# Performance work log

Hardware: AMD Instinct MI355X
Metric: run time of the kernel (lower is better)

The kernel has to match this reference:

```python
import jax, jax.numpy as jnp
import numpy as np

EPS = 1e-5


def gcn_conv(x, W, b, src, dst):
    """PyG GCNConv: transform, add self-loops, symmetric norm, scatter-add, bias."""
    N = x.shape[0]
    h = x @ W  # [N, out]
    loop = jnp.arange(N)
    s = jnp.concatenate([src, loop])  # sources incl. self-loops
    d = jnp.concatenate([dst, loop])  # targets incl. self-loops
    deg = jax.ops.segment_sum(jnp.ones(s.shape[0], h.dtype), d, num_segments=N)
    dis = jnp.where(deg > 0, jax.lax.rsqrt(deg), 0.0)  # deg^-1/2
    norm = dis[s] * dis[d]  # [E+N]
    out = jax.ops.segment_sum(h[s] * norm[:, None], d, num_segments=N)
    return out + b


def batchnorm(x, gamma, beta):
    mu = x.mean(axis=0)
    var = x.var(axis=0)
    return (x - mu) * jax.lax.rsqrt(var + EPS) * gamma + beta


def setup_inputs() -> dict:
    key = jax.random.key(0)
    ks = jax.random.split(key, 6)
    N, E = 100000, 1600000
    IN, HID, OUT = 128, 256, 64
    x = jax.random.normal(ks[0], (N, IN), dtype=jnp.float32)
    edge_index = jax.random.randint(ks[1], (2, E), 0, N, dtype=jnp.int64)
    W1 = jax.random.normal(ks[2], (IN, HID), dtype=jnp.float32) / np.sqrt(IN)
    b1 = jnp.zeros((HID,), jnp.float32)
    gamma1 = jnp.ones((HID,), jnp.float32)
    beta1 = jnp.zeros((HID,), jnp.float32)
    W2 = jax.random.normal(ks[3], (HID, OUT), dtype=jnp.float32) / np.sqrt(HID)
    b2 = jnp.zeros((OUT,), jnp.float32)
    return {"x": x, "edge_index": edge_index, "W1": W1, "b1": b1,
            "gamma1": gamma1, "beta1": beta1, "W2": W2, "b2": b2}


def reference(x, edge_index, W1, b1, gamma1, beta1, W2, b2):
    src, dst = edge_index[0], edge_index[1]
    h = gcn_conv(x, W1, b1, src, dst)
    h = jax.nn.relu(batchnorm(h, gamma1, beta1))
    # dropout is identity at inference
    return gcn_conv(h, W2, b2, src, dst)
```

## Files before the change

kernel.cpp:

```cpp
#include <hip/hip_runtime.h>
#include <hip/hip_bf16.h>


#define IN_F  128
#define HID_F 256
#define OUT_F 64
#define BK_SHIFT 8
#define BK_SIZE  256
#define CHUNK    8192

typedef unsigned int uint;
typedef unsigned short ushort;
typedef short bf16x8 __attribute__((ext_vector_type(8)));
typedef float f32x4 __attribute__((ext_vector_type(4)));

__device__ __forceinline__ ushort f2bf(float f) {
    uint u = __float_as_uint(f);
    uint r = (u + 0x7fffu + ((u >> 16) & 1u)) >> 16;
    return (ushort)r;
}
__device__ __forceinline__ float bf_lo(uint u) { return __uint_as_float(u << 16); }
__device__ __forceinline__ float bf_hi(uint u) { return __uint_as_float(u & 0xffff0000u); }

#define ACC8(u)                                         \
    do {                                                \
        acc[0] += bf_lo((u).x); acc[1] += bf_hi((u).x); \
        acc[2] += bf_lo((u).y); acc[3] += bf_hi((u).y); \
        acc[4] += bf_lo((u).z); acc[5] += bf_hi((u).z); \
        acc[6] += bf_lo((u).w); acc[7] += bf_hi((u).w); \
    } while (0)


__global__ void bucket_hist_kernel(const int* __restrict__ dst, int* __restrict__ bhist,
                                   int E, int NB) {
    __shared__ int h[512];
    for (int i = threadIdx.x; i < NB; i += 256) h[i] = 0;
    __syncthreads();
    int base = blockIdx.x * CHUNK;
    int end = min(base + CHUNK, E);
    for (int i = base + threadIdx.x; i < end; i += 256)
        atomicAdd(&h[dst[i] >> BK_SHIFT], 1);
    __syncthreads();
    for (int i = threadIdx.x; i < NB; i += 256)
        if (h[i]) atomicAdd(&bhist[i], h[i]);
}

__global__ void bucket_scan_kernel(const int* __restrict__ bhist, int* __restrict__ bbase,
                                   int* __restrict__ bcursor, int NB, int E) {
    __shared__ int sh[512];
    int t = threadIdx.x;
    int v = (t < NB) ? bhist[t] : 0;
    sh[t] = v;
    __syncthreads();
    for (int off = 1; off < 512; off <<= 1) {
        int u = (t >= off) ? sh[t - off] : 0;
        __syncthreads();
        sh[t] += u;
        __syncthreads();
    }
    if (t < NB) { int b = sh[t] - v; bbase[t] = b; bcursor[t] = b; }
    if (t == 0) bbase[NB] = E;
}

__global__ void bucket_scatter_kernel(const int* __restrict__ src, const int* __restrict__ dst,
                                      int* __restrict__ bcursor, uint* __restrict__ ebuf,
                                      int E, int NB) {
    __shared__ int h[512];
    __shared__ int cur[512];
    for (int i = threadIdx.x; i < NB; i += 256) h[i] = 0;
    __syncthreads();
    int base = blockIdx.x * CHUNK;
    int end = min(base + CHUNK, E);
    for (int i = base + threadIdx.x; i < end; i += 256)
        atomicAdd(&h[dst[i] >> BK_SHIFT], 1);
    __syncthreads();
    for (int i = threadIdx.x; i < NB; i += 256)
        cur[i] = h[i] ? atomicAdd(&bcursor[i], h[i]) : 0;
    __syncthreads();
    for (int i = base + threadIdx.x; i < end; i += 256) {
        int d = dst[i], s = src[i];
        int b = d >> BK_SHIFT;
        int pos = atomicAdd(&cur[b], 1);
        ebuf[pos] = (uint)s | ((uint)(d & (BK_SIZE - 1)) << 24);
    }
}

__global__ void bucket_build_kernel(const uint* __restrict__ ebuf, const int* __restrict__ bbase,
                                    int* __restrict__ deg_e, int* __restrict__ offsets,
                                    float* __restrict__ dis, int* __restrict__ ssrc, int N) {
    __shared__ int cnt[256], off[256], cur[256];
    int b = blockIdx.x;
    int t = threadIdx.x;
    cnt[t] = 0;
    __syncthreads();
    int e0 = bbase[b], e1 = bbase[b + 1];
    for (int i = e0 + t; i < e1; i += 256)
        atomicAdd(&cnt[ebuf[i] >> 24], 1);
    __syncthreads();
    int v = cnt[t];
    int vpad = (v + 3) & ~3;
    off[t] = vpad;
    __syncthreads();
    for (int o = 1; o < 256; o <<= 1) {
        int u = (t >= o) ? off[t - o] : 0;
        __syncthreads();
        off[t] += u;
        __syncthreads();
    }
    int excl = off[t] - vpad;
    int base_pad = e0 + b * 768;
    int d = b * BK_SIZE + t;
    if (d < N) {
        deg_e[d] = vpad;
        offsets[d] = base_pad + excl;
        dis[d] = rsqrtf((float)(v + 1));
    }
    cur[t] = excl;
    __syncthreads();
    for (int i = e0 + t; i < e1; i += 256) {
        uint e = ebuf[i];
        int ld = e >> 24;
        int pos = atomicAdd(&cur[ld], 1);
        ssrc[base_pad + pos] = (int)(e & 0xFFFFFFu);
    }
    __syncthreads();
    for (int i = v; i < vpad; i++)
        ssrc[base_pad + excl + i] = N;
}

__global__ void prep_kernel(const float* __restrict__ x, const float* __restrict__ dis,
                            uint* __restrict__ xs, const float* __restrict__ W1,
                            const float* __restrict__ W2, ushort* __restrict__ W1bp,
                            ushort* __restrict__ W2bp, int N) {
    int b = blockIdx.x;
    if (b < 192) {
        int i = b * 256 + threadIdx.x;
        if (i < 32768) {
            int kk = i & 31, c = (i >> 5) & 255, kc = i >> 13;
            W1bp[i] = f2bf(W1[(size_t)(kc * 32 + kk) * HID_F + c]);
        } else {
            int j = i - 32768;
            int kk = j & 31, c = (j >> 5) & 63, kc = j >> 11;
            W2bp[j] = f2bf(W2[(size_t)(kc * 32 + kk) * OUT_F + c]);
        }
        return;
    }
    int i = (b - 192) * 256 + threadIdx.x;
    if (i < (N + 1) * (IN_F / 2)) {
        int n = i >> 6;
        if (n >= N) { xs[i] = 0u; return; }
        float dn = dis[n];
        float2 v = ((const float2*)x)[i];
        xs[i] = (uint)f2bf(dn * v.x) | ((uint)f2bf(dn * v.y) << 16);
    }
}


__global__ void aggx_kernel(const uint* __restrict__ xs, const int* __restrict__ ssrc,
                            const int* __restrict__ offsets, const int* __restrict__ deg_e,
                            const float* __restrict__ dis, uint* __restrict__ zb, int N) {
    int lane = threadIdx.x & 63;
    int n = blockIdx.x * 4 + (threadIdx.x >> 6);
    if (n >= N) return;
    int grp = lane >> 4;
    int ck = lane & 15;
    float acc[8];
#pragma unroll
    for (int i = 0; i < 8; i++) acc[i] = 0.f;
    int start = offsets[n], cnt = deg_e[n];
    for (int base = 0; base < cnt; base += 64) {
        int m = min(64, cnt - base);
        int idx = base + lane;
        int sv = ssrc[start + (idx < cnt ? idx : cnt - 1)];
        int rounds = m >> 2;
        int q = 0;
        for (; q + 4 <= rounds; q += 4) {
            int sA = __shfl(sv, ((q + 0) << 2) | grp);
            int sB = __shfl(sv, ((q + 1) << 2) | grp);
            int sC = __shfl(sv, ((q + 2) << 2) | grp);
            int sD = __shfl(sv, ((q + 3) << 2) | grp);
            uint4 uA = *(const uint4*)(xs + ((size_t)sA << 6) + (ck << 2));
            uint4 uB = *(const uint4*)(xs + ((size_t)sB << 6) + (ck << 2));
            uint4 uC = *(const uint4*)(xs + ((size_t)sC << 6) + (ck << 2));
            uint4 uD = *(const uint4*)(xs + ((size_t)sD << 6) + (ck << 2));
            ACC8(uA); ACC8(uB); ACC8(uC); ACC8(uD);
        }
        for (; q < rounds; q++) {
            int s = __shfl(sv, (q << 2) | grp);
            uint4 u = *(const uint4*)(xs + ((size_t)s << 6) + (ck << 2));
            ACC8(u);
        }
    }
#pragma unroll
    for (int i = 0; i < 8; i++) acc[i] += __shfl_down(acc[i], 32);
#pragma unroll
    for (int i = 0; i < 8; i++) acc[i] += __shfl_down(acc[i], 16);
    if (grp == 0) {
        uint4 u = *(const uint4*)(xs + ((size_t)n << 6) + (ck << 2));
        ACC8(u);
        float dn = dis[n];
        uint4 o;
        o.x = (uint)f2bf(dn * acc[0]) | ((uint)f2bf(dn * acc[1]) << 16);
        o.y = (uint)f2bf(dn * acc[2]) | ((uint)f2bf(dn * acc[3]) << 16);
        o.z = (uint)f2bf(dn * acc[4]) | ((uint)f2bf(dn * acc[5]) << 16);
        o.w = (uint)f2bf(dn * acc[6]) | ((uint)f2bf(dn * acc[7]) << 16);
        *(uint4*)(zb + ((size_t)n << 6) + (ck << 2)) = o;
    }
}

__global__ __launch_bounds__(256) void gemm1_kernel(const uint* __restrict__ zb,
                                                    const uint* __restrict__ W1bp,
                                                    const float* __restrict__ b1,
                                                    ushort* __restrict__ out1b,
                                                    float* __restrict__ bnp, int N) {
    __shared__ uint sbuf[8192];
    int t = threadIdx.x;
    int n0 = blockIdx.x * 64;
    for (int i = t; i < 64 * 16; i += 256) {
        int r = i >> 4, q = i & 15;
        int node = n0 + r;
        uint4 v = make_uint4(0u, 0u, 0u, 0u);
        if (node < N) v = *(const uint4*)(zb + (size_t)node * 64 + q * 4);
        int p = q ^ (r & 15);
        *(uint4*)(&sbuf[r * 64 + p * 4]) = v;
    }
    __syncthreads();
    int wave = t >> 6, lane = t & 63;
    int quad = lane >> 4, lrow = lane & 15;
    f32x4 acc[4][4];
#pragma unroll
    for (int m = 0; m < 4; m++)
#pragma unroll
        for (int nt = 0; nt < 4; nt++) acc[m][nt] = (f32x4)(0.f);
#pragma unroll
    for (int kc = 0; kc < 4; kc++) {
        bf16x8 bfr[4];
#pragma unroll
        for (int nt = 0; nt < 4; nt++) {
            int c = wave * 64 + nt * 16 + lrow;
            bfr[nt] = *(const bf16x8*)(W1bp + ((size_t)(kc * 256 + c) * 16 + quad * 4));
        }
        bf16x8 afr[4];
#pragma unroll
        for (int m = 0; m < 4; m++) {
            int p = (kc * 4 + quad) ^ lrow;
            afr[m] = *(const bf16x8*)(&sbuf[(m * 16 + lrow) * 64 + p * 4]);
        }
#pragma unroll
        for (int m = 0; m < 4; m++)
#pragma unroll
            for (int nt = 0; nt < 4; nt++)
                acc[m][nt] = __builtin_amdgcn_mfma_f32_16x16x32_bf16(
                    afr[m], bfr[nt], acc[m][nt], 0, 0, 0);
    }
    __syncthreads();
#pragma unroll
    for (int nt = 0; nt < 4; nt++) {
        int c = wave * 64 + nt * 16 + lrow;
        float bb = b1[c];
        float s = 0.f, q = 0.f;
#pragma unroll
        for (int m = 0; m < 4; m++) {
#pragma unroll
            for (int r = 0; r < 4; r++) {
                int row = m * 16 + quad * 4 + r;
                float v = acc[m][nt][r] + bb;
                if (n0 + row < N) { s += v; q = fmaf(v, v, q); }
                uint hv = (uint)f2bf(v);
                uint pv = __shfl_xor(hv, 1);
                if ((lrow & 1) == 0)
                    sbuf[row * 128 + (c >> 1)] = hv | (pv << 16);
            }
        }
        s += __shfl_down(s, 32); q += __shfl_down(q, 32);
        s += __shfl_down(s, 16); q += __shfl_down(q, 16);
        if (quad == 0) {
            bnp[(size_t)blockIdx.x * 512 + c] = s;
            bnp[(size_t)blockIdx.x * 512 + 256 + c] = q;
        }
    }
    __syncthreads();
    uint* out1g = (uint*)out1b;
    for (int i = t; i < 2048; i += 256) {
        int row = i >> 5;
        if (n0 + row < N)
            *(uint4*)(out1g + (size_t)(n0 + row) * 128 + (i & 31) * 4) =
                *(const uint4*)(&sbuf[i * 4]);
    }
}

__global__ void bnred1_kernel(const float* __restrict__ bnp, float* __restrict__ bnp2,
                              int nblk) {
    int g = blockIdx.x, t = threadIdx.x;
    float s = 0.f, q = 0.f;
    for (int b = g; b < nblk; b += 32) {
        s += bnp[(size_t)b * 512 + t];
        q += bnp[(size_t)b * 512 + 256 + t];
    }
    bnp2[g * 512 + t] = s;
    bnp2[g * 512 + 256 + t] = q;
}

__global__ void bnred2_kernel(const float* __restrict__ bnp2, const float* __restrict__ gamma,
                              const float* __restrict__ beta, float* __restrict__ bnsb, int N) {
    int t = threadIdx.x;
    float s = 0.f, q = 0.f;
    for (int g = 0; g < 32; g++) {
        s += bnp2[g * 512 + t];
        q += bnp2[g * 512 + 256 + t];
    }
    float invN = 1.0f / (float)N;
    float mean = s * invN;
    float var = q * invN - mean * mean;
    float sc = gamma[t] * rsqrtf(fmaxf(var, 0.f) + 1e-5f);
    bnsb[t] = sc;
    bnsb[256 + t] = beta[t] - mean * sc;
}

__global__ __launch_bounds__(256) void gemm2_kernel(const ushort* __restrict__ out1b,
                                                    const uint* __restrict__ W2bp,
                                                    const float* __restrict__ dis,
                                                    const float* __restrict__ bnsb,
                                                    ushort* __restrict__ gs, int N) {
    __shared__ uint sbuf[8192];
    __shared__ float bns[256], bnb[256];
    const uint* out1u = (const uint*)out1b;
    int t = threadIdx.x;
    int n0 = blockIdx.x * 64;
    if (blockIdx.x == 0 && t < 32) ((uint*)gs)[(size_t)N * 32 + t] = 0u;
    bns[t] = bnsb[t];
    bnb[t] = bnsb[256 + t];
    __syncthreads();
    for (int i = t; i < 64 * 32; i += 256) {
        int r = i >> 5, q = i & 31;
        int node = n0 + r;
        uint4 v = make_uint4(0u, 0u, 0u, 0u);
        if (node < N) {
            uint4 w = *(const uint4*)(out1u + (size_t)node * 128 + q * 4);
            int c0 = q * 8;
            float r0 = fmaxf(fmaf(bf_lo(w.x), bns[c0 + 0], bnb[c0 + 0]), 0.f);
            float r1 = fmaxf(fmaf(bf_hi(w.x), bns[c0 + 1], bnb[c0 + 1]), 0.f);
            float r2 = fmaxf(fmaf(bf_lo(w.y), bns[c0 + 2], bnb[c0 + 2]), 0.f);
            float r3 = fmaxf(fmaf(bf_hi(w.y), bns[c0 + 3], bnb[c0 + 3]), 0.f);
            float r4 = fmaxf(fmaf(bf_lo(w.z), bns[c0 + 4], bnb[c0 + 4]), 0.f);
            float r5 = fmaxf(fmaf(bf_hi(w.z), bns[c0 + 5], bnb[c0 + 5]), 0.f);
            float r6 = fmaxf(fmaf(bf_lo(w.w), bns[c0 + 6], bnb[c0 + 6]), 0.f);
            float r7 = fmaxf(fmaf(bf_hi(w.w), bns[c0 + 7], bnb[c0 + 7]), 0.f);
            v.x = (uint)f2bf(r0) | ((uint)f2bf(r1) << 16);
            v.y = (uint)f2bf(r2) | ((uint)f2bf(r3) << 16);
            v.z = (uint)f2bf(r4) | ((uint)f2bf(r5) << 16);
            v.w = (uint)f2bf(r6) | ((uint)f2bf(r7) << 16);
        }
        int p = (q & 16) | ((q & 15) ^ (r & 15));
        *(uint4*)(&sbuf[r * 128 + p * 4]) = v;
    }
    __syncthreads();
    int wave = t >> 6, lane = t & 63;
    int quad = lane >> 4, lrow = lane & 15;
    int c = wave * 16 + lrow;
    f32x4 acc[4];
#pragma unroll
    for (int m = 0; m < 4; m++) acc[m] = (f32x4)(0.f);
#pragma unroll
    for (int kc = 0; kc < 8; kc++) {
        bf16x8 bfr = *(const bf16x8*)(W2bp + ((size_t)(kc * 64 + c) * 16 + quad * 4));
#pragma unroll
        for (int m = 0; m < 4; m++) {
            int q = kc * 4 + quad;
            int p = (q & 16) | ((q & 15) ^ lrow);
            bf16x8 afr = *(const bf16x8*)(&sbuf[(m * 16 + lrow) * 128 + p * 4]);
            acc[m] = __builtin_amdgcn_mfma_f32_16x16x32_bf16(afr, bfr, acc[m], 0, 0, 0);
        }
    }
    __syncthreads();
#pragma unroll
    for (int m = 0; m < 4; m++) {
#pragma unroll
        for (int r = 0; r < 4; r++) {
            int row = m * 16 + quad * 4 + r;
            int node = n0 + row;
            float dn = (node < N) ? dis[node] : 0.f;
            uint hv = (uint)f2bf(dn * acc[m][r]);
            uint pv = __shfl_xor(hv, 1);
            if ((lrow & 1) == 0)
                sbuf[row * 32 + (c >> 1)] = hv | (pv << 16);
        }
    }
    __syncthreads();
    uint* gsg = (uint*)gs;
    for (int i = t; i < 512; i += 256) {
        int row = i >> 3;
        if (n0 + row < N)
            *(uint4*)(gsg + (size_t)(n0 + row) * 32 + (i & 7) * 4) =
                *(const uint4*)(&sbuf[i * 4]);
    }
}

__global__ void agg2_kernel(const uint* __restrict__ gs, const int* __restrict__ ssrc,
                            const int* __restrict__ offsets, const int* __restrict__ deg_e,
                            const float* __restrict__ dis, const float* __restrict__ b2,
                            float* __restrict__ out, int N) {
    int lane = threadIdx.x & 63;
    int n = blockIdx.x * 4 + (threadIdx.x >> 6);
    if (n >= N) return;
    int grp = lane >> 3;
    int ck = lane & 7;
    float acc[8];
#pragma unroll
    for (int i = 0; i < 8; i++) acc[i] = 0.f;
    int start = offsets[n], cnt = deg_e[n];
    for (int base = 0; base < cnt; base += 64) {
        int m = min(64, cnt - base);
        int idx = base + lane;
        int sv = ssrc[start + (idx < cnt ? idx : cnt - 1)];
        int rounds = m >> 3;
        int q = 0;
        for (; q + 2 <= rounds; q += 2) {
            int sA = __shfl(sv, ((q + 0) << 3) | grp);
            int sB = __shfl(sv, ((q + 1) << 3) | grp);
            uint4 uA = *(const uint4*)(gs + ((size_t)sA << 5) + (ck << 2));
            uint4 uB = *(const uint4*)(gs + ((size_t)sB << 5) + (ck << 2));
            ACC8(uA); ACC8(uB);
        }
        for (; q < rounds; q++) {
            int s = __shfl(sv, (q << 3) | grp);
            uint4 u = *(const uint4*)(gs + ((size_t)s << 5) + (ck << 2));
            ACC8(u);
        }
        if (m & 4) {
            int s = __shfl(sv, (rounds << 3) | (grp & 3));
            s = (grp & 4) ? N : s;
            uint4 u = *(const uint4*)(gs + ((size_t)s << 5) + (ck << 2));
            ACC8(u);
        }
    }
#pragma unroll
    for (int i = 0; i < 8; i++) acc[i] += __shfl_down(acc[i], 32);
#pragma unroll
    for (int i = 0; i < 8; i++) acc[i] += __shfl_down(acc[i], 16);
#pragma unroll
    for (int i = 0; i < 8; i++) acc[i] += __shfl_down(acc[i], 8);
    if (grp == 0) {
        uint4 u = *(const uint4*)(gs + ((size_t)n << 5) + (ck << 2));
        ACC8(u);
        float dn = dis[n];
        float4 bb0 = *(const float4*)(b2 + ck * 8);
        float4 bb1 = *(const float4*)(b2 + ck * 8 + 4);
        float* op = out + (size_t)n * OUT_F + ck * 8;
        *(float4*)op = make_float4(fmaf(dn, acc[0], bb0.x), fmaf(dn, acc[1], bb0.y),
                                   fmaf(dn, acc[2], bb0.z), fmaf(dn, acc[3], bb0.w));
        *(float4*)(op + 4) = make_float4(fmaf(dn, acc[4], bb1.x), fmaf(dn, acc[5], bb1.y),
                                         fmaf(dn, acc[6], bb1.z), fmaf(dn, acc[7], bb1.w));
    }
}

extern "C" void kernel_launch(void* const* d_in, const int* in_sizes, int n_in,
                              void* d_out, int out_size, void* d_ws, size_t ws_size,
                              hipStream_t stream) {
    const float* x      = (const float*)d_in[0];
    const int*   edges  = (const int*)d_in[1];
    const float* W1     = (const float*)d_in[2];
    const float* b1     = (const float*)d_in[3];
    const float* gamma1 = (const float*)d_in[4];
    const float* beta1  = (const float*)d_in[5];
    const float* W2     = (const float*)d_in[6];
    const float* b2     = (const float*)d_in[7];
    float* out = (float*)d_out;

    int N = in_sizes[0] / IN_F;
    int E = in_sizes[1] / 2;
    const int* src = edges;
    const int* dst = edges + E;
    int NB = (N + BK_SIZE - 1) / BK_SIZE;
    int nchunks = (E + CHUNK - 1) / CHUNK;
    int nblk1 = (N + 63) / 64;

    char* ws = (char*)d_ws;
    size_t off = 0;
    auto alloc = [&](size_t bytes) -> void* {
        void* p = ws + off;
        off += (bytes + 255) & ~(size_t)255;
        return p;
    };
    int*    deg_e   = (int*)alloc((size_t)N * 4);
    int*    offsets = (int*)alloc((size_t)N * 4);
    float*  dis     = (float*)alloc((size_t)(N + 1) * 4);
    int*    bhist   = (int*)alloc(512 * 4);
    int*    bbase   = (int*)alloc(513 * 4);
    int*    bcursor = (int*)alloc(512 * 4);
    int*    ssrc    = (int*)alloc(((size_t)E + 768 * 512 + 64) * 4);
    uint*   ebuf    = (uint*)alloc((size_t)E * 4);
    uint*   xs      = (uint*)alloc((size_t)(N + 1) * (IN_F / 2) * 4);
    uint*   zb      = (uint*)alloc((size_t)N * (IN_F / 2) * 4);
    ushort* out1b   = (ushort*)alloc((size_t)N * HID_F * 2);
    float*  bnp     = (float*)alloc((size_t)nblk1 * 512 * 4);
    float*  bnp2    = (float*)alloc(32 * 512 * 4);
    float*  bnsb    = (float*)alloc(512 * 4);
    ushort* W1bp    = (ushort*)alloc(4 * 256 * 32 * 2);
    ushort* W2bp    = (ushort*)alloc(8 * 64 * 32 * 2);
    ushort* gs      = (ushort*)zb;

    hipMemsetAsync(bhist, 0, 512 * 4, stream);

    bucket_hist_kernel<<<nchunks, 256, 0, stream>>>(dst, bhist, E, NB);
    bucket_scan_kernel<<<1, 512, 0, stream>>>(bhist, bbase, bcursor, NB, E);
    bucket_scatter_kernel<<<nchunks, 256, 0, stream>>>(src, dst, bcursor, ebuf, E, NB);
    bucket_build_kernel<<<NB, 256, 0, stream>>>(ebuf, bbase, deg_e, offsets, dis, ssrc, N);

    int xblocks = ((N + 1) * (IN_F / 2) + 255) / 256;
    prep_kernel<<<192 + xblocks, 256, 0, stream>>>(x, dis, xs, W1, W2, W1bp, W2bp, N);
    aggx_kernel<<<(N + 3) / 4, 256, 0, stream>>>(xs, ssrc, offsets, deg_e, dis, zb, N);
    gemm1_kernel<<<nblk1, 256, 0, stream>>>(zb, (const uint*)W1bp, b1, out1b, bnp, N);
    bnred1_kernel<<<32, 256, 0, stream>>>(bnp, bnp2, nblk1);
    bnred2_kernel<<<1, 256, 0, stream>>>(bnp2, gamma1, beta1, bnsb, N);
    gemm2_kernel<<<nblk1, 256, 0, stream>>>(out1b, (const uint*)W2bp, dis, bnsb, gs, N);
    agg2_kernel<<<(N + 3) / 4, 256, 0, stream>>>((const uint*)gs, ssrc, offsets, deg_e, dis,
                                                 b2, out, N);
}
```

Measured before the change: 353.6 us.

## Fuse preprocessing and BN reduction kernels to cut launches and passes

Merges the weight bf16 packing into the histogram kernel and the x scaling/conversion into the bucket-build kernel, so x is scaled with degree norms held in shared memory. The two-stage BN reduction becomes one kernel that sums into a global buffer with atomics, and gemm2 now derives the scale and shift itself. CHUNK is doubled, halving the block count for the histogram and scatter kernels. This removes three launches and one full pass, but the build kernel does more per-block work with only NB blocks, and float atomics make the BN sums order-dependent.

```diff
diff --git a/kernel.cpp b/kernel.cpp
--- a/kernel.cpp
+++ b/kernel.cpp
@@ -7,7 +7,7 @@
 #define OUT_F 64
 #define BK_SHIFT 8
 #define BK_SIZE  256
-#define CHUNK    8192
+#define CHUNK    16384
 
 typedef unsigned int uint;
 typedef unsigned short ushort;
@@ -31,110 +31,12 @@
     } while (0)
 
 
-__global__ void bucket_hist_kernel(const int* __restrict__ dst, int* __restrict__ bhist,
-                                   int E, int NB) {
-    __shared__ int h[512];
-    for (int i = threadIdx.x; i < NB; i += 256) h[i] = 0;
-    __syncthreads();
-    int base = blockIdx.x * CHUNK;
-    int end = min(base + CHUNK, E);
-    for (int i = base + threadIdx.x; i < end; i += 256)
-        atomicAdd(&h[dst[i] >> BK_SHIFT], 1);
-    __syncthreads();
-    for (int i = threadIdx.x; i < NB; i += 256)
-        if (h[i]) atomicAdd(&bhist[i], h[i]);
-}
-
-__global__ void bucket_scan_kernel(const int* __restrict__ bhist, int* __restrict__ bbase,
-                                   int* __restrict__ bcursor, int NB, int E) {
-    __shared__ int sh[512];
-    int t = threadIdx.x;
-    int v = (t < NB) ? bhist[t] : 0;
-    sh[t] = v;
-    __syncthreads();
-    for (int off = 1; off < 512; off <<= 1) {
-        int u = (t >= off) ? sh[t - off] : 0;
-        __syncthreads();
-        sh[t] += u;
-        __syncthreads();
-    }
-    if (t < NB) { int b = sh[t] - v; bbase[t] = b; bcursor[t] = b; }
-    if (t == 0) bbase[NB] = E;
-}
-
-__global__ void bucket_scatter_kernel(const int* __restrict__ src, const int* __restrict__ dst,
-                                      int* __restrict__ bcursor, uint* __restrict__ ebuf,
-                                      int E, int NB) {
-    __shared__ int h[512];
-    __shared__ int cur[512];
-    for (int i = threadIdx.x; i < NB; i += 256) h[i] = 0;
-    __syncthreads();
-    int base = blockIdx.x * CHUNK;
-    int end = min(base + CHUNK, E);
-    for (int i = base + threadIdx.x; i < end; i += 256)
-        atomicAdd(&h[dst[i] >> BK_SHIFT], 1);
-    __syncthreads();
-    for (int i = threadIdx.x; i < NB; i += 256)
-        cur[i] = h[i] ? atomicAdd(&bcursor[i], h[i]) : 0;
-    __syncthreads();
-    for (int i = base + threadIdx.x; i < end; i += 256) {
-        int d = dst[i], s = src[i];
-        int b = d >> BK_SHIFT;
-        int pos = atomicAdd(&cur[b], 1);
-        ebuf[pos] = (uint)s | ((uint)(d & (BK_SIZE - 1)) << 24);
-    }
-}
-
-__global__ void bucket_build_kernel(const uint* __restrict__ ebuf, const int* __restrict__ bbase,
-                                    int* __restrict__ deg_e, int* __restrict__ offsets,
-                                    float* __restrict__ dis, int* __restrict__ ssrc, int N) {
-    __shared__ int cnt[256], off[256], cur[256];
-    int b = blockIdx.x;
-    int t = threadIdx.x;
-    cnt[t] = 0;
-    __syncthreads();
-    int e0 = bbase[b], e1 = bbase[b + 1];
-    for (int i = e0 + t; i < e1; i += 256)
-        atomicAdd(&cnt[ebuf[i] >> 24], 1);
-    __syncthreads();
-    int v = cnt[t];
-    int vpad = (v + 3) & ~3;
-    off[t] = vpad;
-    __syncthreads();
-    for (int o = 1; o < 256; o <<= 1) {
-        int u = (t >= o) ? off[t - o] : 0;
-        __syncthreads();
-        off[t] += u;
-        __syncthreads();
-    }
-    int excl = off[t] - vpad;
-    int base_pad = e0 + b * 768;
-    int d = b * BK_SIZE + t;
-    if (d < N) {
-        deg_e[d] = vpad;
-        offsets[d] = base_pad + excl;
-        dis[d] = rsqrtf((float)(v + 1));
-    }
-    cur[t] = excl;
-    __syncthreads();
-    for (int i = e0 + t; i < e1; i += 256) {
-        uint e = ebuf[i];
-        int ld = e >> 24;
-        int pos = atomicAdd(&cur[ld], 1);
-        ssrc[base_pad + pos] = (int)(e & 0xFFFFFFu);
-    }
-    __syncthreads();
-    for (int i = v; i < vpad; i++)
-        ssrc[base_pad + excl + i] = N;
-}
-
-__global__ void prep_kernel(const float* __restrict__ x, const float* __restrict__ dis,
-                            uint* __restrict__ xs, const float* __restrict__ W1,
-                            const float* __restrict__ W2, ushort* __restrict__ W1bp,
-                            ushort* __restrict__ W2bp, int N) {
-    int b = blockIdx.x;
-    if (b < 192) {
-        int i = b * 256 + threadIdx.x;
+__global__ void hist_wprep_kernel(const int* __restrict__ dst, int* __restrict__ bhist,
+                                  const float* __restrict__ W1, const float* __restrict__ W2,
+                                  ushort* __restrict__ W1bp, ushort* __restrict__ W2bp,
+                                  int E, int NB, int nchunk) {
+    if (blockIdx.x >= nchunk) {
+        int i = (blockIdx.x - nchunk) * 256 + threadIdx.x;
         if (i < 32768) {
             int kk = i & 31, c = (i >> 5) & 255, kc = i >> 13;
             W1bp[i] = f2bf(W1[(size_t)(kc * 32 + kk) * HID_F + c]);
@@ -145,13 +47,114 @@
         }
         return;
     }
-    int i = (b - 192) * 256 + threadIdx.x;
-    if (i < (N + 1) * (IN_F / 2)) {
-        int n = i >> 6;
-        if (n >= N) { xs[i] = 0u; return; }
-        float dn = dis[n];
-        float2 v = ((const float2*)x)[i];
-        xs[i] = (uint)f2bf(dn * v.x) | ((uint)f2bf(dn * v.y) << 16);
+    __shared__ int h[512];
+    for (int i = threadIdx.x; i < NB; i += 256) h[i] = 0;
+    __syncthreads();
+    int base = blockIdx.x * CHUNK;
+    int end = min(base + CHUNK, E);
+    for (int i = base + threadIdx.x; i < end; i += 256)
+        atomicAdd(&h[dst[i] >> BK_SHIFT], 1);
+    __syncthreads();
+    for (int i = threadIdx.x; i < NB; i += 256)
+        if (h[i]) atomicAdd(&bhist[i], h[i]);
+}
+
+__global__ void bucket_scan_kernel(const int* __restrict__ bhist, int* __restrict__ bbase,
+                                   int* __restrict__ bcursor, int NB, int E) {
+    __shared__ int sh[512];
+    int t = threadIdx.x;
+    int v = (t < NB) ? bhist[t] : 0;
+    sh[t] = v;
+    __syncthreads();
+    for (int off = 1; off < 512; off <<= 1) {
+        int u = (t >= off) ? sh[t - off] : 0;
+        __syncthreads();
+        sh[t] += u;
+        __syncthreads();
+    }
+    if (t < NB) { int b = sh[t] - v; bbase[t] = b; bcursor[t] = b; }
+    if (t == 0) bbase[NB] = E;
+}
+
+__global__ void bucket_scatter_kernel(const int* __restrict__ src, const int* __restrict__ dst,
+                                      int* __restrict__ bcursor, uint* __restrict__ ebuf,
+                                      int E, int NB) {
+    __shared__ int h[512];
+    __shared__ int cur[512];
+    for (int i = threadIdx.x; i < NB; i += 256) h[i] = 0;
+    __syncthreads();
+    int base = blockIdx.x * CHUNK;
+    int end = min(base + CHUNK, E);
+    for (int i = base + threadIdx.x; i < end; i += 256)
+        atomicAdd(&h[dst[i] >> BK_SHIFT], 1);
+    __syncthreads();
+    for (int i = threadIdx.x; i < NB; i += 256)
+        cur[i] = h[i] ? atomicAdd(&bcursor[i], h[i]) : 0;
+    __syncthreads();
+    for (int i = base + threadIdx.x; i < end; i += 256) {
+        int d = dst[i], s = src[i];
+        int b = d >> BK_SHIFT;
+        int pos = atomicAdd(&cur[b], 1);
+        ebuf[pos] = (uint)s | ((uint)(d & (BK_SIZE - 1)) << 24);
+    }
+}
+
+__global__ void bucket_build_kernel(const uint* __restrict__ ebuf, const int* __restrict__ bbase,
+                                    int* __restrict__ deg_e, int* __restrict__ offsets,
+                                    float* __restrict__ dis, int* __restrict__ ssrc,
+                                    const float* __restrict__ x, uint* __restrict__ xs, int N) {
+    __shared__ int cnt[256], off[256], cur[256];
+    __shared__ float disl[256];
+    int b = blockIdx.x;
+    int t = threadIdx.x;
+    cnt[t] = 0;
+    __syncthreads();
+    int e0 = bbase[b], e1 = bbase[b + 1];
+    for (int i = e0 + t; i < e1; i += 256)
+        atomicAdd(&cnt[ebuf[i] >> 24], 1);
+    __syncthreads();
+    int v = cnt[t];
+    int vpad = (v + 3) & ~3;
+    off[t] = vpad;
+    __syncthreads();
+    for (int o = 1; o < 256; o <<= 1) {
+        int u = (t >= o) ? off[t - o] : 0;
+        __syncthreads();
+        off[t] += u;
+        __syncthreads();
+    }
+    int excl = off[t] - vpad;
+    int base_pad = e0 + b * 768;
+    int d = b * BK_SIZE + t;
+    float dn_t = rsqrtf((float)(v + 1));
+    disl[t] = dn_t;
+    if (d < N) {
+        deg_e[d] = vpad;
+        offsets[d] = base_pad + excl;
+        dis[d] = dn_t;
+    }
+    cur[t] = excl;
+    __syncthreads();
+    for (int i = e0 + t; i < e1; i += 256) {
+        uint e = ebuf[i];
+        int ld = e >> 24;
+        int pos = atomicAdd(&cur[ld], 1);
+        ssrc[base_pad + pos] = (int)(e & 0xFFFFFFu);
+    }
+    for (int i = v; i < vpad; i++)
+        ssrc[base_pad + excl + i] = N;
+    int nbase = b * BK_SIZE;
+    for (int i = t; i < BK_SIZE * 64; i += 256) {
+        int nl = i >> 6, c2 = i & 63;
+        int node = nbase + nl;
+        if (node < N) {
+            float dn = disl[nl];
+            float2 vx = ((const float2*)x)[(size_t)node * 64 + c2];
+            xs[(size_t)node * 64 + c2] =
+                (uint)f2bf(dn * vx.x) | ((uint)f2bf(dn * vx.y) << 16);
+        } else if (node == N) {
+            xs[(size_t)node * 64 + c2] = 0u;
+        }
     }
 }
 
@@ -289,38 +292,24 @@
     }
 }
 
-__global__ void bnred1_kernel(const float* __restrict__ bnp, float* __restrict__ bnp2,
-                              int nblk) {
+__global__ void bnred_kernel(const float* __restrict__ bnp, float* __restrict__ bnsum,
+                             int nblk) {
     int g = blockIdx.x, t = threadIdx.x;
     float s = 0.f, q = 0.f;
     for (int b = g; b < nblk; b += 32) {
         s += bnp[(size_t)b * 512 + t];
         q += bnp[(size_t)b * 512 + 256 + t];
     }
-    bnp2[g * 512 + t] = s;
-    bnp2[g * 512 + 256 + t] = q;
-}
-
-__global__ void bnred2_kernel(const float* __restrict__ bnp2, const float* __restrict__ gamma,
-                              const float* __restrict__ beta, float* __restrict__ bnsb, int N) {
-    int t = threadIdx.x;
-    float s = 0.f, q = 0.f;
-    for (int g = 0; g < 32; g++) {
-        s += bnp2[g * 512 + t];
-        q += bnp2[g * 512 + 256 + t];
-    }
-    float invN = 1.0f / (float)N;
-    float mean = s * invN;
-    float var = q * invN - mean * mean;
-    float sc = gamma[t] * rsqrtf(fmaxf(var, 0.f) + 1e-5f);
-    bnsb[t] = sc;
-    bnsb[256 + t] = beta[t] - mean * sc;
+    atomicAdd(&bnsum[t], s);
+    atomicAdd(&bnsum[256 + t], q);
 }
 
 __global__ __launch_bounds__(256) void gemm2_kernel(const ushort* __restrict__ out1b,
                                                     const uint* __restrict__ W2bp,
                                                     const float* __restrict__ dis,
-                                                    const float* __restrict__ bnsb,
+                                                    const float* __restrict__ bnsum,
+                                                    const float* __restrict__ gamma,
+                                                    const float* __restrict__ beta,
                                                     ushort* __restrict__ gs, int N) {
     __shared__ uint sbuf[8192];
     __shared__ float bns[256], bnb[256];
@@ -328,8 +317,14 @@
     int t = threadIdx.x;
     int n0 = blockIdx.x * 64;
     if (blockIdx.x == 0 && t < 32) ((uint*)gs)[(size_t)N * 32 + t] = 0u;
-    bns[t] = bnsb[t];
-    bnb[t] = bnsb[256 + t];
+    {
+        float invN = 1.0f / (float)N;
+        float mean = bnsum[t] * invN;
+        float var = bnsum[256 + t] * invN - mean * mean;
+        float sc = gamma[t] * rsqrtf(fmaxf(var, 0.f) + 1e-5f);
+        bns[t] = sc;
+        bnb[t] = beta[t] - mean * sc;
+    }
     __syncthreads();
     for (int i = t; i < 64 * 32; i += 256) {
         int r = i >> 5, q = i & 31;
@@ -486,6 +481,7 @@
     int*    offsets = (int*)alloc((size_t)N * 4);
     float*  dis     = (float*)alloc((size_t)(N + 1) * 4);
     int*    bhist   = (int*)alloc(512 * 4);
+    float*  bnsum   = (float*)alloc(512 * 4);
     int*    bbase   = (int*)alloc(513 * 4);
     int*    bcursor = (int*)alloc(512 * 4);
     int*    ssrc    = (int*)alloc(((size_t)E + 768 * 512 + 64) * 4);
@@ -494,26 +490,23 @@
     uint*   zb      = (uint*)alloc((size_t)N * (IN_F / 2) * 4);
     ushort* out1b   = (ushort*)alloc((size_t)N * HID_F * 2);
     float*  bnp     = (float*)alloc((size_t)nblk1 * 512 * 4);
-    float*  bnp2    = (float*)alloc(32 * 512 * 4);
-    float*  bnsb    = (float*)alloc(512 * 4);
     ushort* W1bp    = (ushort*)alloc(4 * 256 * 32 * 2);
     ushort* W2bp    = (ushort*)alloc(8 * 64 * 32 * 2);
     ushort* gs      = (ushort*)zb;
 
-    hipMemsetAsync(bhist, 0, 512 * 4, stream);
-
-    bucket_hist_kernel<<<nchunks, 256, 0, stream>>>(dst, bhist, E, NB);
+    hipMemsetAsync(bhist, 0, 2 * 512 * 4, stream);
+
+    hist_wprep_kernel<<<nchunks + 192, 256, 0, stream>>>(dst, bhist, W1, W2, W1bp, W2bp,
+                                                         E, NB, nchunks);
     bucket_scan_kernel<<<1, 512, 0, stream>>>(bhist, bbase, bcursor, NB, E);
     bucket_scatter_kernel<<<nchunks, 256, 0, stream>>>(src, dst, bcursor, ebuf, E, NB);
-    bucket_build_kernel<<<NB, 256, 0, stream>>>(ebuf, bbase, deg_e, offsets, dis, ssrc, N);
-
-    int xblocks = ((N + 1) * (IN_F / 2) + 255) / 256;
-    prep_kernel<<<192 + xblocks, 256, 0, stream>>>(x, dis, xs, W1, W2, W1bp, W2bp, N);
+    bucket_build_kernel<<<NB, 256, 0, stream>>>(ebuf, bbase, deg_e, offsets, dis, ssrc,
+                                                x, xs, N);
     aggx_kernel<<<(N + 3) / 4, 256, 0, stream>>>(xs, ssrc, offsets, deg_e, dis, zb, N);
     gemm1_kernel<<<nblk1, 256, 0, stream>>>(zb, (const uint*)W1bp, b1, out1b, bnp, N);
-    bnred1_kernel<<<32, 256, 0, stream>>>(bnp, bnp2, nblk1);
-    bnred2_kernel<<<1, 256, 0, stream>>>(bnp2, gamma1, beta1, bnsb, N);
-    gemm2_kernel<<<nblk1, 256, 0, stream>>>(out1b, (const uint*)W2bp, dis, bnsb, gs, N);
+    bnred_kernel<<<32, 256, 0, stream>>>(bnp, bnsum, nblk1);
+    gemm2_kernel<<<nblk1, 256, 0, stream>>>(out1b, (const uint*)W2bp, dis, bnsum,
+                                            gamma1, beta1, gs, N);
     agg2_kernel<<<(N + 3) / 4, 256, 0, stream>>>((const uint*)gs, ssrc, offsets, deg_e, dis,
                                                  b2, out, N);
 }
```

After: 405.0 us. 1.15x slower.
